# Performance work log

Measured on AMD Instinct MI355X. Metric: run time of the kernel, lower is better.

Reference implementation:

```python
import jax, jax.numpy as jnp
import numpy as np

B, N, F, K = 512, 128, 128, 4


def setup_inputs() -> dict:
    key = jax.random.key(0)
    ks = jax.random.split(key, 12)
    # xavier-normal-ish scales
    s_rw = float(np.sqrt(2.0 / (F + F)))
    s_sw = float(np.sqrt(2.0 / (F + F)))
    inp = {
        "H": jax.random.normal(ks[0], (B, N, F), dtype=jnp.float32),
        "E": jax.random.uniform(ks[1], (B, N, N, K), dtype=jnp.float32),
        "RW1": jax.random.normal(ks[2], (F, F, K), dtype=jnp.float32) * s_rw,
        "SW1": jax.random.normal(ks[3], (F, F), dtype=jnp.float32) * s_sw,
        "RW2": jax.random.normal(ks[4], (F, F, K), dtype=jnp.float32) * s_rw,
        "SW2": jax.random.normal(ks[5], (F, F), dtype=jnp.float32) * s_sw,
        "RW3": jax.random.normal(ks[6], (F, F, K), dtype=jnp.float32) * s_rw,
        "SW3": jax.random.normal(ks[7], (F, F), dtype=jnp.float32) * s_sw,
        "W1": jax.random.normal(ks[8], (F, 20), dtype=jnp.float32) * float(np.sqrt(1.0 / F)),
        "b1": jnp.zeros((20,), dtype=jnp.float32),
        "W2": jax.random.normal(ks[9], (20, 1), dtype=jnp.float32) * float(np.sqrt(1.0 / 20)),
        "b2": jnp.zeros((1,), dtype=jnp.float32),
    }
    return inp


def _rgcn_conv(H, E, D, RW, SW):
    # einsum('bi,bijk,bjm,mnk->bin') done in two GEMM-shaped steps
    M = jnp.einsum('bijk,bjm->bimk', E, H)          # [B,N,F,K]
    msg = jnp.einsum('bimk,mnk->bin', M, RW)        # [B,N,F]
    return jax.nn.sigmoid(msg * D[:, :, None] + jnp.einsum('bij,jl->bil', H, SW))


def reference(H, E, RW1, SW1, RW2, SW2, RW3, SW3, W1, b1, W2, b2):
    # degree norm with self-loops: (E + eye)[b,i,:,:].sum() = E.sum((2,3)) + K
    k = jnp.asarray(E.shape[-1], dtype=E.dtype)
    D = 1.0 / (E.sum(axis=(2, 3)) + k)              # [B,N]
    H = _rgcn_conv(H, E, D, RW1, SW1)
    H = _rgcn_conv(H, E, D, RW2, SW2)
    H = _rgcn_conv(H, E, D, RW3, SW3)
    h = jnp.maximum(H @ W1 + b1, 0.1 * (H @ W1 + b1))  # LeakyReLU(0.1)
    score = jnp.mean(jax.nn.sigmoid(h @ W2 + b2))
    return score
```

## Files before the change

kernel.cpp:

```cpp
#include <hip/hip_runtime.h>
#include <math.h>

#define BB 512
#define NN 128
#define FF 128
#define KK 4

typedef __attribute__((ext_vector_type(8))) short bf16x8;
typedef __attribute__((ext_vector_type(4))) float f32x4;

__device__ inline unsigned short f2bf(float x) {
  union { float f; unsigned int u; } v; v.f = x;
  unsigned int r = v.u + 0x7fff + ((v.u >> 16) & 1);
  return (unsigned short)(r >> 16);
}
__device__ inline float bf2f(unsigned short h) {
  union { unsigned int u; float f; } v; v.u = ((unsigned int)h) << 16; return v.f;
}

__global__ __launch_bounds__(256) void k_convE(const float* __restrict__ E,
                                               unsigned short* __restrict__ Eb,
                                               float* __restrict__ Dv) {
  int wave = threadIdx.x >> 6;
  int lane = threadIdx.x & 63;
  int row  = blockIdx.x * 4 + wave;
  const float* p = E + (size_t)row * 512 + lane * 8;
  f32x4 a = *(const f32x4*)p;
  f32x4 b = *(const f32x4*)(p + 4);
  float s = a[0] + a[1] + a[2] + a[3] + b[0] + b[1] + b[2] + b[3];
  #pragma unroll
  for (int off = 32; off > 0; off >>= 1) s += __shfl_down(s, off, 64);
  if (lane == 0) Dv[row] = 1.0f / (s + 4.0f);
  union { unsigned short h[8]; f32x4 v; } u;
  u.h[0] = f2bf(a[0]); u.h[1] = f2bf(a[1]); u.h[2] = f2bf(a[2]); u.h[3] = f2bf(a[3]);
  u.h[4] = f2bf(b[0]); u.h[5] = f2bf(b[1]); u.h[6] = f2bf(b[2]); u.h[7] = f2bf(b[3]);
  *(f32x4*)(Eb + (size_t)row * 512 + lane * 8) = u.v;
}

__global__ __launch_bounds__(256) void k_convH(const float* __restrict__ H,
                                               unsigned short* __restrict__ Hb) {
  size_t i = ((size_t)blockIdx.x * 256 + threadIdx.x) * 8;
  f32x4 a = *(const f32x4*)(H + i);
  f32x4 b = *(const f32x4*)(H + i + 4);
  union { unsigned short h[8]; f32x4 v; } u;
  u.h[0] = f2bf(a[0]); u.h[1] = f2bf(a[1]); u.h[2] = f2bf(a[2]); u.h[3] = f2bf(a[3]);
  u.h[4] = f2bf(b[0]); u.h[5] = f2bf(b[1]); u.h[6] = f2bf(b[2]); u.h[7] = f2bf(b[3]);
  *(f32x4*)(Hb + i) = u.v;
}

__global__ __launch_bounds__(256) void k_buildW(const float* __restrict__ RW,
                                                const float* __restrict__ SW,
                                                unsigned short* __restrict__ W2) {
  int idx = blockIdx.x * 256 + threadIdx.x;
  int m = idx & 127;
  int c = idx >> 7;
  float v = (c < 512) ? RW[m * 512 + c] : SW[m * 128 + (c - 512)];
  W2[idx] = f2bf(v);
}

#define GS_PITCH 132

__global__ __launch_bounds__(512, 4) void k_layer(
    const unsigned short* __restrict__ Eb,
    const unsigned short* __restrict__ Hin,
    const unsigned short* __restrict__ W2L,
    const float* __restrict__ Dv,
    unsigned short* __restrict__ Hout)
{
  __shared__ unsigned short Gs[128 * GS_PITCH];

  const int b = blockIdx.x;
  const unsigned short* E_b = Eb  + (size_t)b * 65536;
  const unsigned short* H_b = Hin + (size_t)b * 16384;

  const int tid = threadIdx.x;
  const int w = tid >> 6, l = tid & 63;
  const int wr = w >> 1, wc = w & 1;
  const int lq = l >> 4, lm = l & 15;

  f32x4 macc[2][4] = {};
  bf16x8 pa[2];

  #pragma unroll
  for (int s = 0; s < 4; ++s) {
    if (s) __syncthreads();

    #pragma unroll
    for (int f = 0; f < 2; ++f)
      pa[f] = *(const bf16x8*)(E_b + (wr * 32 + f * 16 + lm) * 512 + s * 128 + lq * 8);

    f32x4 gacc[4][2] = {};
    #pragma unroll
    for (int k0 = 0; k0 < 128; k0 += 32) {
      bf16x8 fa[4], fb[2];
      #pragma unroll
      for (int f = 0; f < 4; ++f)
        fa[f] = *(const bf16x8*)(W2L + (w * 64 + f * 16 + lm) * 128 + k0 + lq * 8);
      #pragma unroll
      for (int g = 0; g < 2; ++g)
        fb[g] = *(const bf16x8*)(H_b + (s * 32 + g * 16 + lm) * 128 + k0 + lq * 8);
      #pragma unroll
      for (int f = 0; f < 4; ++f)
        #pragma unroll
        for (int g = 0; g < 2; ++g)
          gacc[f][g] = __builtin_amdgcn_mfma_f32_16x16x32_bf16(fa[f], fb[g], gacc[f][g], 0, 0, 0);
    }
    #pragma unroll
    for (int f = 0; f < 4; ++f) {
      int n = w * 16 + f * 4 + lq;
      #pragma unroll
      for (int g = 0; g < 2; ++g) {
        int jl = g * 16 + lm;
        union { unsigned short h4[4]; uint2 v; } u;
        u.h4[0] = f2bf(gacc[f][g][0]); u.h4[1] = f2bf(gacc[f][g][1]);
        u.h4[2] = f2bf(gacc[f][g][2]); u.h4[3] = f2bf(gacc[f][g][3]);
        *(uint2*)(&Gs[n * GS_PITCH + jl * 4]) = u.v;
      }
    }
    __syncthreads();

    #pragma unroll
    for (int kt = 0; kt < 4; ++kt) {
      bf16x8 fb[4];
      #pragma unroll
      for (int g = 0; g < 4; ++g)
        fb[g] = *(const bf16x8*)(&Gs[(wc * 64 + g * 16 + lm) * GS_PITCH + kt * 32 + lq * 8]);
      bf16x8 na[2];
      if (kt < 3) {
        #pragma unroll
        for (int f = 0; f < 2; ++f)
          na[f] = *(const bf16x8*)(E_b + (wr * 32 + f * 16 + lm) * 512 + s * 128 + (kt + 1) * 32 + lq * 8);
      }
      #pragma unroll
      for (int f = 0; f < 2; ++f)
        #pragma unroll
        for (int g = 0; g < 4; ++g)
          macc[f][g] = __builtin_amdgcn_mfma_f32_16x16x32_bf16(pa[f], fb[g], macc[f][g], 0, 0, 0);
      if (kt < 3) { pa[0] = na[0]; pa[1] = na[1]; }
    }
  }

  f32x4 sacc[2][4] = {};
  #pragma unroll
  for (int k0 = 0; k0 < 128; k0 += 32) {
    bf16x8 fa[2], fb[4];
    #pragma unroll
    for (int f = 0; f < 2; ++f)
      fa[f] = *(const bf16x8*)(H_b + (wr * 32 + f * 16 + lm) * 128 + k0 + lq * 8);
    #pragma unroll
    for (int g = 0; g < 4; ++g)
      fb[g] = *(const bf16x8*)(W2L + (512 + wc * 64 + g * 16 + lm) * 128 + k0 + lq * 8);
    #pragma unroll
    for (int f = 0; f < 2; ++f)
      #pragma unroll
      for (int g = 0; g < 4; ++g)
        sacc[f][g] = __builtin_amdgcn_mfma_f32_16x16x32_bf16(fa[f], fb[g], sacc[f][g], 0, 0, 0);
  }

  const float* dvb = Dv + b * 128;
  unsigned short* O_b = Hout + (size_t)b * 16384;
  #pragma unroll
  for (int f = 0; f < 2; ++f) {
    int i0 = wr * 32 + f * 16 + lq * 4;
    f32x4 d = *(const f32x4*)(dvb + i0);
    #pragma unroll
    for (int g = 0; g < 4; ++g) {
      int n = wc * 64 + g * 16 + lm;
      #pragma unroll
      for (int r = 0; r < 4; ++r) {
        float v = fmaf(macc[f][g][r], d[r], sacc[f][g][r]);
        O_b[(i0 + r) * 128 + n] = f2bf(1.0f / (1.0f + __expf(-v)));
      }
    }
  }
}

__global__ __launch_bounds__(256) void k_mlp(
    const unsigned short* __restrict__ H,
    const float* __restrict__ W1,
    const float* __restrict__ b1,
    const float* __restrict__ W2,
    const float* __restrict__ b2,
    float* __restrict__ sumOut)
{
  __shared__ float W1s[128 * 20];
  __shared__ float b1s[20], W2s[20];
  __shared__ float red[256];
  for (int i = threadIdx.x; i < 2560; i += 256) W1s[i] = W1[i];
  if (threadIdx.x < 20) { b1s[threadIdx.x] = b1[threadIdx.x]; W2s[threadIdx.x] = W2[threadIdx.x]; }
  __syncthreads();

  int row = blockIdx.x * 256 + threadIdx.x;
  float h[20];
  #pragma unroll
  for (int j = 0; j < 20; ++j) h[j] = b1s[j];
  const unsigned short* hr = H + (size_t)row * 128;
  for (int m8 = 0; m8 < 128; m8 += 8) {
    f32x4 pk = *(const f32x4*)(hr + m8);
    const unsigned short* us = (const unsigned short*)&pk;
    #pragma unroll
    for (int e = 0; e < 8; ++e) {
      float x = bf2f(us[e]);
      #pragma unroll
      for (int j = 0; j < 20; ++j) h[j] = fmaf(x, W1s[(m8 + e) * 20 + j], h[j]);
    }
  }
  float v = b2[0];
  #pragma unroll
  for (int j = 0; j < 20; ++j) {
    float t = h[j];
    t = fmaxf(t, 0.1f * t);
    v = fmaf(t, W2s[j], v);
  }
  float s = 1.0f / (1.0f + __expf(-v));

  red[threadIdx.x] = s;
  __syncthreads();
  #pragma unroll
  for (int off = 128; off > 0; off >>= 1) {
    if (threadIdx.x < off) red[threadIdx.x] += red[threadIdx.x + off];
    __syncthreads();
  }
  if (threadIdx.x == 0) atomicAdd(sumOut, red[0]);
}

__global__ void k_final(const float* __restrict__ sum, float* __restrict__ out) {
  out[0] = sum[0] * (1.0f / 65536.0f);
}

extern "C" void kernel_launch(void* const* d_in, const int* in_sizes, int n_in,
                              void* d_out, int out_size, void* d_ws, size_t ws_size,
                              hipStream_t stream) {
  const float* H   = (const float*)d_in[0];
  const float* E   = (const float*)d_in[1];
  const float* RW1 = (const float*)d_in[2];
  const float* SW1 = (const float*)d_in[3];
  const float* RW2 = (const float*)d_in[4];
  const float* SW2 = (const float*)d_in[5];
  const float* RW3 = (const float*)d_in[6];
  const float* SW3 = (const float*)d_in[7];
  const float* W1  = (const float*)d_in[8];
  const float* b1  = (const float*)d_in[9];
  const float* W2  = (const float*)d_in[10];
  const float* b2  = (const float*)d_in[11];
  float* out = (float*)d_out;

  char* w = (char*)d_ws;
  float*          wsD   = (float*)w;           w += (size_t)65536 * 4;
  unsigned short* wsEb  = (unsigned short*)w;  w += (size_t)33554432 * 2;
  unsigned short* wsHa  = (unsigned short*)w;  w += (size_t)8388608 * 2;
  unsigned short* wsHb  = (unsigned short*)w;  w += (size_t)8388608 * 2;
  unsigned short* wsW2  = (unsigned short*)w;  w += (size_t)3 * 81920 * 2;
  float*          wsSum = (float*)w;           w += 256;

  k_convE<<<BB * NN / 4, 256, 0, stream>>>(E, wsEb, wsD);
  k_convH<<<8388608 / (256 * 8), 256, 0, stream>>>(H, wsHa);
  k_buildW<<<320, 256, 0, stream>>>(RW1, SW1, wsW2);
  k_buildW<<<320, 256, 0, stream>>>(RW2, SW2, wsW2 + 81920);
  k_buildW<<<320, 256, 0, stream>>>(RW3, SW3, wsW2 + 163840);
  hipMemsetAsync(wsSum, 0, sizeof(float), stream);

  k_layer<<<BB, 512, 0, stream>>>(wsEb, wsHa, wsW2,          wsD, wsHb);
  k_layer<<<BB, 512, 0, stream>>>(wsEb, wsHb, wsW2 + 81920,  wsD, wsHa);
  k_layer<<<BB, 512, 0, stream>>>(wsEb, wsHa, wsW2 + 163840, wsD, wsHb);

  k_mlp<<<BB * NN / 256, 256, 0, stream>>>(wsHb, W1, b1, W2, b2, wsSum);
  k_final<<<1, 1, 0, stream>>>(wsSum, out);
}
```

Before: 501.6 us.

## Stage E tiles into swizzled LDS via async global_load_lds and coalesce output stores

The layer kernel now copies each 128x128 E slice into a new XOR-swizzled shared buffer with asynchronous global-to-LDS loads. The copy is issued before the G GEMM so it overlaps that compute, replacing the per-kt register prefetch of E from global memory. The first k-step of W/H operands is hoisted ahead of the copy. The output tile is also staged through LDS and written with wide contiguous stores instead of scattered 2-byte stores. This adds 32KB of shared memory per block, which may lower occupancy under launch_bounds(512,4), and adds extra barriers.

```diff
diff --git a/kernel.cpp b/kernel.cpp
--- a/kernel.cpp
+++ b/kernel.cpp
@@ -16,6 +16,12 @@
 }
 __device__ inline float bf2f(unsigned short h) {
   union { unsigned int u; float f; } v; v.u = ((unsigned int)h) << 16; return v.f;
+}
+
+__device__ inline void g2l16(const unsigned short* gptr, unsigned short* lptr) {
+  __builtin_amdgcn_global_load_lds(
+      (const __attribute__((address_space(1))) unsigned int*)gptr,
+      (__attribute__((address_space(3))) unsigned int*)lptr, 16, 0, 0);
 }
 
 __global__ __launch_bounds__(256) void k_convE(const float* __restrict__ E,
@@ -68,6 +74,7 @@
     unsigned short* __restrict__ Hout)
 {
   __shared__ unsigned short Gs[128 * GS_PITCH];
+  __shared__ unsigned short Es[128 * 128];
 
   const int b = blockIdx.x;
   const unsigned short* E_b = Eb  + (size_t)b * 65536;
@@ -79,19 +86,34 @@
   const int lq = l >> 4, lm = l & 15;
 
   f32x4 macc[2][4] = {};
-  bf16x8 pa[2];
-
-  #pragma unroll
+
   for (int s = 0; s < 4; ++s) {
     if (s) __syncthreads();
 
-    #pragma unroll
-    for (int f = 0; f < 2; ++f)
-      pa[f] = *(const bf16x8*)(E_b + (wr * 32 + f * 16 + lm) * 512 + s * 128 + lq * 8);
+    bf16x8 fa0[4], fb0[2];
+    #pragma unroll
+    for (int f = 0; f < 4; ++f)
+      fa0[f] = *(const bf16x8*)(W2L + (w * 64 + f * 16 + lm) * 128 + lq * 8);
+    #pragma unroll
+    for (int g = 0; g < 2; ++g)
+      fb0[g] = *(const bf16x8*)(H_b + (s * 32 + g * 16 + lm) * 128 + lq * 8);
+
+    #pragma unroll
+    for (int r = 0; r < 4; ++r) {
+      int R   = r * 32 + w * 4 + (l >> 4);
+      int cbg = (l & 15) ^ (R & 15);
+      g2l16(E_b + R * 512 + s * 128 + cbg * 8,
+            Es + (r * 32 + w * 4) * 128);
+    }
 
     f32x4 gacc[4][2] = {};
     #pragma unroll
-    for (int k0 = 0; k0 < 128; k0 += 32) {
+    for (int f = 0; f < 4; ++f)
+      #pragma unroll
+      for (int g = 0; g < 2; ++g)
+        gacc[f][g] = __builtin_amdgcn_mfma_f32_16x16x32_bf16(fa0[f], fb0[g], gacc[f][g], 0, 0, 0);
+    #pragma unroll
+    for (int k0 = 32; k0 < 128; k0 += 32) {
       bf16x8 fa[4], fb[2];
       #pragma unroll
       for (int f = 0; f < 4; ++f)
@@ -121,22 +143,21 @@
 
     #pragma unroll
     for (int kt = 0; kt < 4; ++kt) {
-      bf16x8 fb[4];
+      bf16x8 ea[2], fb[4];
+      #pragma unroll
+      for (int f = 0; f < 2; ++f) {
+        int i  = wr * 32 + f * 16 + lm;
+        int cb = (kt * 4 + lq) ^ lm;
+        ea[f] = *(const bf16x8*)(Es + i * 128 + cb * 8);
+      }
       #pragma unroll
       for (int g = 0; g < 4; ++g)
         fb[g] = *(const bf16x8*)(&Gs[(wc * 64 + g * 16 + lm) * GS_PITCH + kt * 32 + lq * 8]);
-      bf16x8 na[2];
-      if (kt < 3) {
-        #pragma unroll
-        for (int f = 0; f < 2; ++f)
-          na[f] = *(const bf16x8*)(E_b + (wr * 32 + f * 16 + lm) * 512 + s * 128 + (kt + 1) * 32 + lq * 8);
-      }
       #pragma unroll
       for (int f = 0; f < 2; ++f)
         #pragma unroll
         for (int g = 0; g < 4; ++g)
-          macc[f][g] = __builtin_amdgcn_mfma_f32_16x16x32_bf16(pa[f], fb[g], macc[f][g], 0, 0, 0);
-      if (kt < 3) { pa[0] = na[0]; pa[1] = na[1]; }
+          macc[f][g] = __builtin_amdgcn_mfma_f32_16x16x32_bf16(ea[f], fb[g], macc[f][g], 0, 0, 0);
     }
   }
 
@@ -158,7 +179,7 @@
   }
 
   const float* dvb = Dv + b * 128;
-  unsigned short* O_b = Hout + (size_t)b * 16384;
+  __syncthreads();
   #pragma unroll
   for (int f = 0; f < 2; ++f) {
     int i0 = wr * 32 + f * 16 + lq * 4;
@@ -169,9 +190,22 @@
       #pragma unroll
       for (int r = 0; r < 4; ++r) {
         float v = fmaf(macc[f][g][r], d[r], sacc[f][g][r]);
-        O_b[(i0 + r) * 128 + n] = f2bf(1.0f / (1.0f + __expf(-v)));
+        Es[(i0 + r) * 128 + n] = f2bf(1.0f / (1.0f + __expf(-v)));
       }
     }
+  }
+  __syncthreads();
+  unsigned short* O_b = Hout + (size_t)b * 16384;
+  {
+    int off = tid * 32;
+    f32x4 v0 = *(const f32x4*)(Es + off);
+    f32x4 v1 = *(const f32x4*)(Es + off + 8);
+    f32x4 v2 = *(const f32x4*)(Es + off + 16);
+    f32x4 v3 = *(const f32x4*)(Es + off + 24);
+    *(f32x4*)(O_b + off)      = v0;
+    *(f32x4*)(O_b + off + 8)  = v1;
+    *(f32x4*)(O_b + off + 16) = v2;
+    *(f32x4*)(O_b + off + 24) = v3;
   }
 }
 
```

New measurement: 514.1 us. 1.02x slower.
